# Kernel optimization log

Measured on AMD Instinct MI355X. Metric: run time of the kernel, lower is better.

The kernel has to match this reference:

```python
import jax, jax.numpy as jnp
import numpy as np
from jax import lax

B, T, HW = 8, 32, 128
D, NH, DEPTH, DFF = 384, 6, 6, 1536
PR = PC = 4
P = PR * PC
EPS = 1e-5


def _ln(x, g, b):
    mu = x.mean(-1, keepdims=True)
    v = ((x - mu) ** 2).mean(-1, keepdims=True)
    return (x - mu) / jnp.sqrt(v + EPS) * g + b


def _conv2d(x, w, s, p):
    return lax.conv_general_dilated(x, w, (s, s), [(p, p), (p, p)],
                                    dimension_numbers=('NCHW', 'OIHW', 'NCHW'))


def _bn(x, g, b, m, v):
    inv = g / jnp.sqrt(v + EPS)
    return x * inv[:, None, None] + (b - m * inv)[:, None, None]


def _gelu(x):
    return jax.nn.gelu(x, approximate=False)


def _forward(frames, conv1_w, bn1_g, bn1_b, bn1_m, bn1_v,
             conv2_w, bn2_g, bn2_b, bn2_m, bn2_v,
             conv3_w, bn3_g, bn3_b, bn3_m, bn3_v, proj_w,
             dw_w, dw_b, pw_w, pw_b, tnorm_g, tnorm_b,
             frame_pos, patch_pos, cls_token, cls_pos,
             qkv_w, qkv_b, out_w, out_b, ln1_g, ln1_b, ln2_g, ln2_b,
             ffn_w1, ffn_b1, ffn_w2, ffn_b2,
             head_ln_g, head_ln_b, head_w1, head_b1, head_w2, head_b2):
    b, t = frames.shape[0], frames.shape[1]
    # ---- FrameEncoder (eval-mode BN) ----
    x = frames.reshape(b * t, 1, HW, HW)
    x = _gelu(_bn(_conv2d(x, conv1_w, 2, 2), bn1_g, bn1_b, bn1_m, bn1_v))
    x = _gelu(_bn(_conv2d(x, conv2_w, 2, 1), bn2_g, bn2_b, bn2_m, bn2_v))
    x = _gelu(_bn(_conv2d(x, conv3_w, 2, 1), bn3_g, bn3_b, bn3_m, bn3_v))
    n, c, hh, ww = x.shape
    # adaptive avg pool (16,16)->(4,4) is an exact 4x4 mean pool
    x = x.reshape(n, c, PR, hh // PR, PC, ww // PC).mean(axis=(3, 5))
    x = jnp.einsum('oc,nchw->nohw', proj_w[:, :, 0, 0], x)  # 1x1 conv proj
    tokens = x.reshape(n, D, P).transpose(0, 2, 1).reshape(b, t, P, D)
    # ---- TemporalConvBlock (per-patch sequences) ----
    tc = tokens.transpose(0, 2, 1, 3).reshape(b * P, t, D)
    out = tc.transpose(0, 2, 1)  # [N, D, t]
    for i, dil in enumerate((1, 2)):
        pad = dil * (3 - 1) // 2
        h = lax.conv_general_dilated(out, dw_w[i], (1,), [(pad, pad)],
                                     rhs_dilation=(dil,), feature_group_count=D,
                                     dimension_numbers=('NCH', 'OIH', 'NCH'))
        h = _gelu(h + dw_b[i][None, :, None])
        h = jnp.einsum('oi,nit->not', pw_w[i], h) + pw_b[i][None, :, None]
        out = h + out
    out = out.transpose(0, 2, 1)
    tc = _ln(out + tc, tnorm_g, tnorm_b)
    tokens = tc.reshape(b, P, t, D).transpose(0, 2, 1, 3)
    # ---- positional + cls ----
    fp = frame_pos[:t].transpose(1, 0, 2)[:, :, None, :]  # [1,t,1,D]
    pp = patch_pos[:, None, :, :]                          # [1,1,P,D]
    tok = (tokens + fp + pp).reshape(b, t * P, D)
    cls = cls_token + cls_pos
    tok = jnp.concatenate([jnp.broadcast_to(cls, (b, 1, D)), tok], axis=1)
    S = t * P + 1
    # ---- block-structured additive mask (faithful to _build_causal_mask) ----
    ids = jnp.repeat(jnp.arange(t), P)
    neg = jnp.finfo(jnp.float32).min
    base = jnp.where(ids[None, :] < ids[:, None], neg, 0.0)
    mask = jnp.zeros((S, S), jnp.float32).at[1:, 1:].set(base).at[1:, 0].set(neg)
    # ---- pre-norm transformer encoder ----
    hd = D // NH
    scale = 1.0 / jnp.sqrt(jnp.float32(hd))
    x = tok
    for i in range(DEPTH):
        h = _ln(x, ln1_g[i], ln1_b[i])
        qkv = h @ qkv_w[i].T + qkv_b[i]
        q, k, v = jnp.split(qkv, 3, axis=-1)
        q = q.reshape(b, S, NH, hd).transpose(0, 2, 1, 3)
        k = k.reshape(b, S, NH, hd).transpose(0, 2, 1, 3)
        v = v.reshape(b, S, NH, hd).transpose(0, 2, 1, 3)
        scores = jnp.einsum('bhqd,bhkd->bhqk', q, k) * scale + mask
        a = jax.nn.softmax(scores, axis=-1)
        o = jnp.einsum('bhqk,bhkd->bhqd', a, v).transpose(0, 2, 1, 3).reshape(b, S, D)
        x = x + (o @ out_w[i].T + out_b[i])
        h2 = _ln(x, ln2_g[i], ln2_b[i])
        x = x + _gelu(h2 @ ffn_w1[i].T + ffn_b1[i]) @ ffn_w2[i].T + ffn_b2[i]
    # ---- coord head ----
    pooled = x[:, 0]
    h = _ln(pooled, head_ln_g, head_ln_b)
    h = _gelu(h @ head_w1.T + head_b1)
    coords = jax.nn.sigmoid(h @ head_w2.T + head_b2)
    return coords


def setup_inputs():
    ks = iter(jax.random.split(jax.random.key(0), 64))

    def r(shape, s):
        return jax.random.normal(next(ks), shape, jnp.float32) * s

    inp = {}
    inp['frames'] = jax.random.normal(next(ks), (B, T, 1, HW, HW), jnp.float32)
    inp['conv1_w'] = r((32, 1, 5, 5), 0.2)
    inp['bn1_g'] = jnp.ones(32); inp['bn1_b'] = jnp.zeros(32)
    inp['bn1_m'] = r((32,), 0.1)
    inp['bn1_v'] = jax.random.uniform(next(ks), (32,), jnp.float32, 0.5, 1.5)
    inp['conv2_w'] = r((64, 32, 3, 3), 0.1)
    inp['bn2_g'] = jnp.ones(64); inp['bn2_b'] = jnp.zeros(64)
    inp['bn2_m'] = r((64,), 0.1)
    inp['bn2_v'] = jax.random.uniform(next(ks), (64,), jnp.float32, 0.5, 1.5)
    inp['conv3_w'] = r((128, 64, 3, 3), 0.07)
    inp['bn3_g'] = jnp.ones(128); inp['bn3_b'] = jnp.zeros(128)
    inp['bn3_m'] = r((128,), 0.1)
    inp['bn3_v'] = jax.random.uniform(next(ks), (128,), jnp.float32, 0.5, 1.5)
    inp['proj_w'] = r((D, 128, 1, 1), 0.08)
    inp['dw_w'] = r((2, D, 1, 3), 0.3)
    inp['dw_b'] = jnp.zeros((2, D))
    inp['pw_w'] = r((2, D, D), 0.05)
    inp['pw_b'] = jnp.zeros((2, D))
    inp['tnorm_g'] = jnp.ones(D); inp['tnorm_b'] = jnp.zeros(D)
    inp['frame_pos'] = r((T, 1, D), 0.02)
    inp['patch_pos'] = r((1, P, D), 0.02)
    inp['cls_token'] = jnp.zeros((1, 1, D))
    inp['cls_pos'] = r((1, 1, D), 0.02)
    inp['qkv_w'] = r((DEPTH, 3 * D, D), 0.02)
    inp['qkv_b'] = jnp.zeros((DEPTH, 3 * D))
    inp['out_w'] = r((DEPTH, D, D), 0.02)
    inp['out_b'] = jnp.zeros((DEPTH, D))
    inp['ln1_g'] = jnp.ones((DEPTH, D)); inp['ln1_b'] = jnp.zeros((DEPTH, D))
    inp['ln2_g'] = jnp.ones((DEPTH, D)); inp['ln2_b'] = jnp.zeros((DEPTH, D))
    inp['ffn_w1'] = r((DEPTH, DFF, D), 0.02)
    inp['ffn_b1'] = jnp.zeros((DEPTH, DFF))
    inp['ffn_w2'] = r((DEPTH, D, DFF), 0.02)
    inp['ffn_b2'] = jnp.zeros((DEPTH, D))
    inp['head_ln_g'] = jnp.ones(D); inp['head_ln_b'] = jnp.zeros(D)
    inp['head_w1'] = r((D, D), 0.02); inp['head_b1'] = jnp.zeros(D)
    inp['head_w2'] = r((2, D), 0.02); inp['head_b2'] = jnp.zeros(2)
    return inp


def reference(frames, conv1_w, bn1_g, bn1_b, bn1_m, bn1_v,
              conv2_w, bn2_g, bn2_b, bn2_m, bn2_v,
              conv3_w, bn3_g, bn3_b, bn3_m, bn3_v, proj_w,
              dw_w, dw_b, pw_w, pw_b, tnorm_g, tnorm_b,
              frame_pos, patch_pos, cls_token, cls_pos,
              qkv_w, qkv_b, out_w, out_b, ln1_g, ln1_b, ln2_g, ln2_b,
              ffn_w1, ffn_b1, ffn_w2, ffn_b2,
              head_ln_g, head_ln_b, head_w1, head_b1, head_w2, head_b2):
    return _forward(frames, conv1_w, bn1_g, bn1_b, bn1_m, bn1_v,
                    conv2_w, bn2_g, bn2_b, bn2_m, bn2_v,
                    conv3_w, bn3_g, bn3_b, bn3_m, bn3_v, proj_w,
                    dw_w, dw_b, pw_w, pw_b, tnorm_g, tnorm_b,
                    frame_pos, patch_pos, cls_token, cls_pos,
                    qkv_w, qkv_b, out_w, out_b, ln1_g, ln1_b, ln2_g, ln2_b,
                    ffn_w1, ffn_b1, ffn_w2, ffn_b2,
                    head_ln_g, head_ln_b, head_w1, head_b1, head_w2, head_b2)
```

## Files before the change

### kernel.cpp

```cpp
#include <hip/hip_runtime.h>
#include <hip/hip_fp16.h>
#include <cstddef>

#define EPSV 1e-5f
#define SPLITS 4

typedef _Float16 f16;
typedef _Float16 f16x8 __attribute__((ext_vector_type(8)));
typedef float f32x4v __attribute__((ext_vector_type(4)));

__device__ __forceinline__ float gelu_f(float x) {
    return 0.5f * x * (1.0f + erff(x * 0.7071067811865476f));
}

__device__ __forceinline__ float gelu_fast(float x) {
    float x2 = x * x;
    float z = x * fmaf(0.10296103f, x2, 2.3025851f);
    float e = exp2f(z);
    float r = __builtin_amdgcn_rcpf(e + 1.0f);
    return fmaf(-x, r, x);
}

__global__ __launch_bounds__(256) void cvt_all_kernel(
    const float* __restrict__ p0, const float* __restrict__ p1,
// ... 162 lines not shown
        f16x8 b0 = *(const f16x8*)(&Bs[(wc + l15) * 40 + l4 * 8]);
        f16x8 b1 = *(const f16x8*)(&Bs[(wc + 16 + l15) * 40 + l4 * 8]);
        acc[0][0] = __builtin_amdgcn_mfma_f32_16x16x32_f16(a0, b0, acc[0][0], 0, 0, 0);
        acc[0][1] = __builtin_amdgcn_mfma_f32_16x16x32_f16(a0, b1, acc[0][1], 0, 0, 0);
        acc[1][0] = __builtin_amdgcn_mfma_f32_16x16x32_f16(a1, b0, acc[1][0], 0, 0, 0);
        acc[1][1] = __builtin_amdgcn_mfma_f32_16x16x32_f16(a1, b1, acc[1][1], 0, 0, 0);
    }
    float inv[2], beta[2];
    #pragma unroll
    for (int ni = 0; ni < 2; ni++) {
        int col = bn + wc + ni * 16 + l15;
        float iv = g[col] * rsqrtf(vr[col] + EPSV);
        inv[ni] = iv; beta[ni] = bt[col] - mn[col] * iv;
    }
    #pragma unroll
    for (int mi = 0; mi < 2; mi++) {
        #pragma unroll
        for (int q = 0; q < 4; q++) {
            int pixel = bm + wr + mi * 16 + l4 * 4 + q;
            #pragma unroll
            for (int ni = 0; ni < 2; ni++) {
                int col = bn + wc + ni * 16 + l15;
                float v = acc[mi][ni][q] * inv[ni] + beta[ni];
                out[(size_t)pixel * CO + col] = (f16)gelu_fast(v);
            }
        }
    }
}

__global__ __launch_bounds__(256) void poolh_kernel(
    const f16* __restrict__ in, f16* __restrict__ out, int NC)
{
    int idx = blockIdx.x * 256 + threadIdx.x;
    if (idx >= NC * 16 * 16) return;
    int cc = idx & 15; int npl = idx >> 4;
    int c0 = cc * 8;
    int n = npl >> 4; int p = npl & 15;
    int ph = p >> 2, pw = p & 3;
    const f16* base = in + (((size_t)(n * 16 + ph * 4)) * 16 + pw * 4) * 128 + c0;
    float s[8] = {};
    #pragma unroll
    for (int dy = 0; dy < 4; dy++)
        #pragma unroll
        for (int dx = 0; dx < 4; dx++) {
            f16x8 v = *(const f16x8*)(base + (dy * 16 + dx) * 128);
            #pragma unroll
            for (int u = 0; u < 8; u++) s[u] += (float)v[u];
        }
    f16* op = out + (size_t)npl * 128 + c0;
    #pragma unroll
    for (int u = 0; u < 8; u++) op[u] = (f16)(s[u] * 0.0625f);
}

template<int OUTF16, int ACT, int VTRANS, int TCMAP>
__global__ __launch_bounds__(256) void gemm_k64_kernel(
    const f16* __restrict__ A, const f16* __restrict__ B,
    const float* __restrict__ bias, const float* __restrict__ res,
    void* __restrict__ Cv, f16* __restrict__ vT, int M, int N, int K, int nrow)
{
    __shared__ __align__(16) f16 As[64 * 72];
    __shared__ __align__(16) f16 Bs[64 * 72];
    int nb = gridDim.x;
    int q = nb >> 3, r = nb & 7;
    int xcd = blockIdx.x & 7, pos = blockIdx.x >> 3;
    int logical = (xcd < r ? xcd * (q + 1) : r * (q + 1) + (xcd - r) * q) + pos;
    int brow = logical % nrow, bcol = logical / nrow;
    int bm = brow * 64, bn = bcol * 64;

    int tid = threadIdx.x;
    int lrow = tid >> 2, lseg = (tid & 3) * 16;
    int w = tid >> 6, lane = tid & 63;
    int wr = (w >> 1) * 32, wc = (w & 1) * 32;
    int l15 = lane & 15, l4 = lane >> 4;
    f32x4v zero = {0.f, 0.f, 0.f, 0.f};
    f32x4v acc[2][2];
    acc[0][0] = zero; acc[0][1] = zero; acc[1][0] = zero; acc[1][1] = zero;

    int arow = bm + lrow;
    bool aok = (arow < M);
    const f16* ap = A + (size_t)arow * K + lseg;
    const f16* bp = B + (size_t)(bn + lrow) * K + lseg;

    uint4 ra0 = make_uint4(0u,0u,0u,0u), ra1 = ra0, rb0, rb1;
    if (aok) { ra0 = *(const uint4*)(ap); ra1 = *(const uint4*)(ap + 8); }
    rb0 = *(const uint4*)(bp); rb1 = *(const uint4*)(bp + 8);

    int nt = K >> 6;
    for (int t = 0; t < nt; t++) {
        __syncthreads();
        *(uint4*)(&As[lrow * 72 + lseg])     = ra0;
        *(uint4*)(&As[lrow * 72 + lseg + 8]) = ra1;
        *(uint4*)(&Bs[lrow * 72 + lseg])     = rb0;
        *(uint4*)(&Bs[lrow * 72 + lseg + 8]) = rb1;
        if (t + 1 < nt) {
            int k0 = (t + 1) << 6;
            if (aok) { ra0 = *(const uint4*)(ap + k0); ra1 = *(const uint4*)(ap + k0 + 8); }
            rb0 = *(const uint4*)(bp + k0); rb1 = *(const uint4*)(bp + k0 + 8);
        }
        __syncthreads();
        #pragma unroll
        for (int s = 0; s < 2; s++) {
            f16x8 a0 = *(const f16x8*)(&As[(wr + l15) * 72 + s * 32 + l4 * 8]);
            f16x8 a1 = *(const f16x8*)(&As[(wr + 16 + l15) * 72 + s * 32 + l4 * 8]);
            f16x8 b0 = *(const f16x8*)(&Bs[(wc + l15) * 72 + s * 32 + l4 * 8]);
            f16x8 b1 = *(const f16x8*)(&Bs[(wc + 16 + l15) * 72 + s * 32 + l4 * 8]);
            acc[0][0] = __builtin_amdgcn_mfma_f32_16x16x32_f16(a0, b0, acc[0][0], 0, 0, 0);
            acc[0][1] = __builtin_amdgcn_mfma_f32_16x16x32_f16(a0, b1, acc[0][1], 0, 0, 0);
            acc[1][0] = __builtin_amdgcn_mfma_f32_16x16x32_f16(a1, b0, acc[1][0], 0, 0, 0);
            acc[1][1] = __builtin_amdgcn_mfma_f32_16x16x32_f16(a1, b1, acc[1][1], 0, 0, 0);
        }
    }

    if (VTRANS && bn >= 768) {
        __syncthreads();
        f16* tile = As;
        #pragma unroll
        for (int mi = 0; mi < 2; mi++)
            #pragma unroll
            for (int qq = 0; qq < 4; qq++) {
                int rl = wr + mi * 16 + l4 * 4 + qq;
                #pragma unroll
                for (int ni = 0; ni < 2; ni++) {
                    int dl = wc + ni * 16 + l15;
                    float v = acc[mi][ni][qq] + bias[bn + dl];
                    tile[dl * 66 + rl] = (f16)v;
                }
            }
        __syncthreads();
        int h = (bn - 768) >> 6;
        int j = tid & 63, dbase = tid >> 6;
        int trow = bm + j;
        if (trow < M) {
            int b = trow / 513;
            int jj = trow - b * 513;
            f16* vb = vT + ((size_t)(b * 6 + h) * 64) * 576 + jj;
            #pragma unroll
            for (int it = 0; it < 16; it++) {
                int d = dbase * 16 + it;
                vb[(size_t)d * 576] = tile[d * 66 + j];
            }
        }
        return;
    }
    #pragma unroll
    for (int mi = 0; mi < 2; mi++) {
        #pragma unroll
        for (int qq = 0; qq < 4; qq++) {
            int row = bm + wr + mi * 16 + l4 * 4 + qq;
            if (row >= M) continue;
            #pragma unroll
            for (int ni = 0; ni < 2; ni++) {
                int col = bn + wc + ni * 16 + l15;
                float v = acc[mi][ni][qq];
                if (bias) v += bias[col];
                if (ACT == 1) v = gelu_fast(v);
                if (res) v += res[(size_t)row * N + col];
                int orow = row;
                if (TCMAP) orow = (row & ~511) | ((row & 15) << 5) | ((row >> 4) & 31);
                if (OUTF16) ((f16*)Cv)[(size_t)orow * N + col] = (f16)v;
                else ((float*)Cv)[(size_t)orow * N + col] = v;
            }
        }
    }
}

template<int ACT>
__global__ __launch_bounds__(256) void gemm_kn128_kernel(
    const f16* __restrict__ A, const f16* __restrict__ B,
    const float* __restrict__ bias, f16* __restrict__ C,
    int M, int N, int K, int nrow)
{
    __shared__ __align__(16) f16 As[64 * 72];
    __shared__ __align__(16) f16 Bs[128 * 72];
    int nb = gridDim.x;
    int q = nb >> 3, r = nb & 7;
    int xcd = blockIdx.x & 7, pos = blockIdx.x >> 3;
    int logical = (xcd < r ? xcd * (q + 1) : r * (q + 1) + (xcd - r) * q) + pos;
    int brow = logical % nrow, bcol = logical / nrow;
    int bm = brow * 64, bn = bcol * 128;

    int tid = threadIdx.x;
    int w = tid >> 6, lane = tid & 63;
    int wr = (w >> 1) * 32, wc = (w & 1) * 64;
    int l15 = lane & 15, l4 = lane >> 4;
    int alrow = tid >> 2, alseg = (tid & 3) * 16;
    int blrow = tid >> 1, blseg = (tid & 1) * 32;

    f32x4v zero = {0.f, 0.f, 0.f, 0.f};
    f32x4v acc[2][4];
    #pragma unroll
    for (int i = 0; i < 2; i++)
        #pragma unroll
        for (int j = 0; j < 4; j++) acc[i][j] = zero;

    int arow = bm + alrow;
    bool aok = (arow < M);
    const f16* ap = A + (size_t)arow * K + alseg;
    const f16* bp = B + (size_t)(bn + blrow) * K + blseg;

    uint4 ra0 = make_uint4(0u,0u,0u,0u), ra1 = ra0;
    uint4 rb0, rb1, rb2, rb3;
    if (aok) { ra0 = *(const uint4*)(ap); ra1 = *(const uint4*)(ap + 8); }
    rb0 = *(const uint4*)(bp);      rb1 = *(const uint4*)(bp + 8);
    rb2 = *(const uint4*)(bp + 16); rb3 = *(const uint4*)(bp + 24);

    int ntiles = K >> 6;
    for (int t = 0; t < ntiles; t++) {
        __syncthreads();
        *(uint4*)(&As[alrow * 72 + alseg])     = ra0;
        *(uint4*)(&As[alrow * 72 + alseg + 8]) = ra1;
        *(uint4*)(&Bs[blrow * 72 + blseg])      = rb0;
        *(uint4*)(&Bs[blrow * 72 + blseg + 8])  = rb1;
        *(uint4*)(&Bs[blrow * 72 + blseg + 16]) = rb2;
        *(uint4*)(&Bs[blrow * 72 + blseg + 24]) = rb3;
        if (t + 1 < ntiles) {
            int k0 = (t + 1) << 6;
            if (aok) { ra0 = *(const uint4*)(ap + k0); ra1 = *(const uint4*)(ap + k0 + 8); }
            rb0 = *(const uint4*)(bp + k0);      rb1 = *(const uint4*)(bp + k0 + 8);
            rb2 = *(const uint4*)(bp + k0 + 16); rb3 = *(const uint4*)(bp + k0 + 24);
        }
        __syncthreads();
        #pragma unroll
        for (int s = 0; s < 2; s++) {
            f16x8 a0 = *(const f16x8*)(&As[(wr + l15) * 72 + s * 32 + l4 * 8]);
            f16x8 a1 = *(const f16x8*)(&As[(wr + 16 + l15) * 72 + s * 32 + l4 * 8]);
            #pragma unroll
            for (int j = 0; j < 4; j++) {
                f16x8 bf = *(const f16x8*)(&Bs[(wc + j * 16 + l15) * 72 + s * 32 + l4 * 8]);
                acc[0][j] = __builtin_amdgcn_mfma_f32_16x16x32_f16(a0, bf, acc[0][j], 0, 0, 0);
                acc[1][j] = __builtin_amdgcn_mfma_f32_16x16x32_f16(a1, bf, acc[1][j], 0, 0, 0);
            }
        }
    }
    #pragma unroll
    for (int mi = 0; mi < 2; mi++) {
        #pragma unroll
        for (int qq = 0; qq < 4; qq++) {
            int row = bm + wr + mi * 16 + l4 * 4 + qq;
            if (row >= M) continue;
            #pragma unroll
            for (int j = 0; j < 4; j++) {
                int col = bn + wc + j * 16 + l15;
                float v = acc[mi][j][qq];
                if (bias) v += bias[col];
                if (ACT == 1) v = gelu_fast(v);
                C[(size_t)row * N + col] = (f16)v;
            }
        }
    }
}

__global__ __launch_bounds__(256) void dwconv_kernel(
    const float* __restrict__ in, const float* __restrict__ w,
    const float* __restrict__ bias, f16* __restrict__ out, int dil)
{
    int idx = blockIdx.x * 256 + threadIdx.x;
    if (idx >= 128 * 32 * 384) return;
    int d = idx % 384; int t = (idx / 384) & 31; int s = idx / (384 * 32);
    const float* ip = in + (size_t)s * 32 * 384 + d;
    float acc = bias[d];
    #pragma unroll
    for (int k = 0; k < 3; k++) {
        int tt = t + (k - 1) * dil;
        if ((unsigned)tt < 32u) acc += w[d * 3 + k] * ip[tt * 384];
    }
    out[idx] = (f16)gelu_fast(acc);
}

__global__ __launch_bounds__(256) void ln_wave_kernel(
    const float* __restrict__ in,
    const float* __restrict__ g, const float* __restrict__ b,
    f16* __restrict__ out, int rows)
{
    int w = threadIdx.x >> 6, lane = threadIdx.x & 63;
    int row = blockIdx.x * 4 + w;
    if (row >= rows) return;
    const float* ip = in + (size_t)row * 384;
    float x[6]; float s = 0.f, s2 = 0.f;
    #pragma unroll
    for (int k = 0; k < 6; k++) {
        float v = ip[lane + 64 * k];
        x[k] = v; s += v; s2 += v * v;
    }
    #pragma unroll
    for (int off = 1; off < 64; off <<= 1) {
        s += __shfl_xor(s, off); s2 += __shfl_xor(s2, off);
    }
    float mu = s * (1.f / 384.f);
    float var = s2 * (1.f / 384.f) - mu * mu;
    float rs = rsqrtf(var + EPSV);
    #pragma unroll
    for (int k = 0; k < 6; k++) {
        int c = lane + 64 * k;
        out[(size_t)row * 384 + c] = (f16)((x[k] - mu) * rs * g[c] + b[c]);
    }
}

__global__ __launch_bounds__(128) void build_x_kernel(
    const float* __restrict__ mix, const float* __restrict__ tc,
    const float* __restrict__ tg, const float* __restrict__ tb,
    const float* __restrict__ fpos, const float* __restrict__ ppos,
    float* __restrict__ x)
{
    int row = blockIdx.x;
    int t = row & 31; int bp = row >> 5;
    int p = bp & 15; int b = bp >> 4;
    int tid = threadIdx.x;
    const float* ip = mix + (size_t)row * 384;
    const float* ip2 = tc + (size_t)row * 384;
    __shared__ float red[128], red2[128];
    float v[3]; float s = 0.f, s2 = 0.f;
    #pragma unroll
    for (int j = 0; j < 3; j++) {
        float val = ip[tid + 128 * j] + ip2[tid + 128 * j];
        v[j] = val; s += val; s2 += val * val;
    }
    red[tid] = s; red2[tid] = s2; __syncthreads();
    for (int off = 64; off >= 1; off >>= 1) {
        if (tid < off) { red[tid] += red[tid + off]; red2[tid] += red2[tid + off]; }
        __syncthreads();
    }
    float mu = red[0] * (1.f / 384.f);
    float var = red2[0] * (1.f / 384.f) - mu * mu;
    float rs = rsqrtf(var + EPSV);
    size_t xbase = ((size_t)b * 513 + 1 + t * 16 + p) * 384;
    #pragma unroll
    for (int j = 0; j < 3; j++) {
        int c = tid + 128 * j;
        float y = (v[j] - mu) * rs * tg[c] + tb[c] + fpos[t * 384 + c] + ppos[p * 384 + c];
        x[xbase + c] = y;
    }
}

__global__ __launch_bounds__(256) void cls_kernel(
    const float* __restrict__ ct, const float* __restrict__ cp, float* __restrict__ x)
{
    int idx = blockIdx.x * 256 + threadIdx.x;
    if (idx >= 8 * 384) return;
    int c = idx % 384; int b = idx / 384;
    x[(size_t)b * 513 * 384 + c] = ct[c] + cp[c];
}

__global__ __launch_bounds__(256) void fattn_split_kernel(
    const f16* __restrict__ qkv, const f16* __restrict__ vT,
    f16* __restrict__ Op, float* __restrict__ ml)
{
    __shared__ __align__(16) f16 Pl[4][16][72];
    int qt = blockIdx.x;
// ... 75 lines not shown
                float sv = valid ? S[jf][r] * 0.125f : -INFINITY;
                pj[jf][r] = sv;
                mx = fmaxf(mx, sv);
            }
            mx = fmaxf(mx, __shfl_xor(mx, 1));
            mx = fmaxf(mx, __shfl_xor(mx, 2));
            mx = fmaxf(mx, __shfl_xor(mx, 4));
            mx = fmaxf(mx, __shfl_xor(mx, 8));
            float mn = fmaxf(m[r], mx);
            float alpha = (m[r] == -INFINITY) ? 0.f : __expf(m[r] - mn);
            float ls = 0.f;
            #pragma unroll
            for (int jf = 0; jf < 4; jf++) {
                float p = (pj[jf][r] == -INFINITY) ? 0.f : __expf(pj[jf][r] - mn);
                pj[jf][r] = p; ls += p;
            }
            ls += __shfl_xor(ls, 1); ls += __shfl_xor(ls, 2);
            ls += __shfl_xor(ls, 4); ls += __shfl_xor(ls, 8);
            l[r] = alpha * l[r] + ls;
            m[r] = mn;
            #pragma unroll
            for (int df = 0; df < 4; df++) O[df][r] *= alpha;
        }
        #pragma unroll
        for (int jf = 0; jf < 4; jf++)
            #pragma unroll
            for (int r = 0; r < 4; r++)
                Pl[w][4 * g + r][jf * 16 + l15] = (f16)pj[jf][r];
        #pragma unroll
        for (int s = 0; s < 2; s++) {
            f16x8 pf = *(const f16x8*)(&Pl[w][l15][s * 32 + g * 8]);
            #pragma unroll
            for (int df = 0; df < 4; df++)
                O[df] = __builtin_amdgcn_mfma_f32_16x16x32_f16(pf, vreg[s * 4 + df], O[df], 0, 0, 0);
        }
        #pragma unroll
        for (int i = 0; i < 8; i++) kreg[i] = knext[i];
    }

    int rowbase = third * 24624 + bh * 513;
    #pragma unroll
    for (int r = 0; r < 4; r++) {
        int qi = q0w + 4 * g + r;
        if (qi > 512) continue;
        size_t ro = (size_t)(rowbase + qi);
        #pragma unroll
        for (int df = 0; df < 4; df++)
            Op[ro * 64 + df * 16 + l15] = (f16)O[df][r];
        if (l15 == 0) {
            ml[ro * 2 + 0] = m[r];
            ml[ro * 2 + 1] = l[r];
        }
    }
}

__global__ __launch_bounds__(256) void attn_combine_kernel(
    const f16* __restrict__ Op, const float* __restrict__ ml,
    f16* __restrict__ ob)
{
    int row = blockIdx.x * 4 + (threadIdx.x >> 6);
    if (row >= 24624) return;
    int lane = threadIdx.x & 63;
    int bh = row / 513, qi = row - bh * 513;
    int b = bh / 6, h = bh - b * 6;
    float mv[SPLITS], lv[SPLITS], mm = -INFINITY;
    #pragma unroll
    for (int s = 0; s < SPLITS; s++) {
        mv[s] = ml[((size_t)s * 24624 + row) * 2];
        lv[s] = ml[((size_t)s * 24624 + row) * 2 + 1];
        mm = fmaxf(mm, mv[s]);
    }
    float onum = 0.f, lden = 0.f;
    #pragma unroll
    for (int s = 0; s < SPLITS; s++) {
        float a = (mv[s] == -INFINITY) ? 0.f : __expf(mv[s] - mm);
        lden += lv[s] * a;
        onum += (float)Op[((size_t)s * 24624 + row) * 64 + lane] * a;
    }
    ob[((size_t)(b * 513 + qi)) * 384 + h * 64 + lane] = (f16)(onum / lden);
}

__global__ __launch_bounds__(384) void head_kernel(
    const float* __restrict__ x, const float* __restrict__ lg, const float* __restrict__ lb,
    const float* __restrict__ w1, const float* __restrict__ b1,
    const float* __restrict__ w2, const float* __restrict__ b2,
    float* __restrict__ out)
{
    int b = blockIdx.x; int t = threadIdx.x;
    __shared__ float hs[384], h1[384];
    __shared__ float rs[6], rs2[6];
    const float* xp = x + (size_t)b * 513 * 384;
    float v = xp[t];
    float s = v, s2 = v * v;
    #pragma unroll
    for (int off = 32; off >= 1; off >>= 1) {
        s += __shfl_down(s, off); s2 += __shfl_down(s2, off);
    }
    if ((t & 63) == 0) { rs[t >> 6] = s; rs2[t >> 6] = s2; }
    __syncthreads();
    float S = 0.f, S2 = 0.f;
    #pragma unroll
    for (int i = 0; i < 6; i++) { S += rs[i]; S2 += rs2[i]; }
    float mu = S * (1.f / 384.f);
    float var = S2 * (1.f / 384.f) - mu * mu;
    float rstd = rsqrtf(var + EPSV);
    hs[t] = (v - mu) * rstd * lg[t] + lb[t];
    __syncthreads();
    const float* wr = w1 + (size_t)t * 384;
    float acc = b1[t];
    for (int c = 0; c < 384; c += 4) {
        float4 w4 = *reinterpret_cast<const float4*>(wr + c);
        acc += w4.x * hs[c] + w4.y * hs[c + 1] + w4.z * hs[c + 2] + w4.w * hs[c + 3];
    }
    h1[t] = gelu_f(acc);
    __syncthreads();
    float p0 = h1[t] * w2[t], p1 = h1[t] * w2[384 + t];
    #pragma unroll
    for (int off = 32; off >= 1; off >>= 1) {
        p0 += __shfl_down(p0, off); p1 += __shfl_down(p1, off);
    }
    if ((t & 63) == 0) { rs[t >> 6] = p0; rs2[t >> 6] = p1; }
    __syncthreads();
    if (t == 0) {
        float a0 = b2[0], a1 = b2[1];
        #pragma unroll
        for (int i = 0; i < 6; i++) { a0 += rs[i]; a1 += rs2[i]; }
        out[b * 2 + 0] = 1.f / (1.f + expf(-a0));
        out[b * 2 + 1] = 1.f / (1.f + expf(-a1));
    }
}

static inline int cdiv(int a, int b) { return (a + b - 1) / b; }
// ... 8 lines not shown
    const float* bn1_m = (const float*)d_in[4]; const float* bn1_v = (const float*)d_in[5];
    const float* conv2_w = (const float*)d_in[6];
    const float* bn2_g = (const float*)d_in[7]; const float* bn2_b = (const float*)d_in[8];
    const float* bn2_m = (const float*)d_in[9]; const float* bn2_v = (const float*)d_in[10];
    const float* conv3_w = (const float*)d_in[11];
    const float* bn3_g = (const float*)d_in[12]; const float* bn3_b = (const float*)d_in[13];
    const float* bn3_m = (const float*)d_in[14]; const float* bn3_v = (const float*)d_in[15];
    const float* proj_w = (const float*)d_in[16];
    const float* dw_w = (const float*)d_in[17]; const float* dw_b = (const float*)d_in[18];
    const float* pw_w = (const float*)d_in[19]; const float* pw_b = (const float*)d_in[20];
    const float* tnorm_g = (const float*)d_in[21]; const float* tnorm_b = (const float*)d_in[22];
    const float* frame_pos = (const float*)d_in[23];
    const float* patch_pos = (const float*)d_in[24];
    const float* cls_token = (const float*)d_in[25];
    const float* cls_pos = (const float*)d_in[26];
    const float* qkv_w = (const float*)d_in[27]; const float* qkv_b = (const float*)d_in[28];
    const float* out_w = (const float*)d_in[29]; const float* out_b = (const float*)d_in[30];
    const float* ln1_g = (const float*)d_in[31]; const float* ln1_b = (const float*)d_in[32];
    const float* ln2_g = (const float*)d_in[33]; const float* ln2_b = (const float*)d_in[34];
    const float* ffn_w1 = (const float*)d_in[35]; const float* ffn_b1 = (const float*)d_in[36];
    const float* ffn_w2 = (const float*)d_in[37]; const float* ffn_b2 = (const float*)d_in[38];
    const float* head_ln_g = (const float*)d_in[39]; const float* head_ln_b = (const float*)d_in[40];
    const float* head_w1 = (const float*)d_in[41]; const float* head_b1 = (const float*)d_in[42];
    const float* head_w2 = (const float*)d_in[43]; const float* head_b2 = (const float*)d_in[44];
    (void)in_sizes; (void)n_in; (void)out_size; (void)ws_size;

    char* base = (char*)d_ws;
    size_t off = 0;
    auto alloc = [&](size_t bytes) { void* p = base + off; off = (off + bytes + 255) & ~(size_t)255; return p; };

    f16* wtotal = (f16*)alloc((size_t)10960896 * 2);
    f16* projw16 = wtotal;
    f16* pw16    = wtotal + 49152;
    f16* qkvw16  = wtotal + 344064;
    f16* outw16  = wtotal + 2998272;
    f16* f1w16   = wtotal + 3883008;
    f16* f2w16   = wtotal + 7421952;
    f16* c1wB    = (f16*)alloc(1024 * 2);
    f16* c2w16   = (f16*)alloc((size_t)64 * 288 * 2);
    f16* c3w16   = (f16*)alloc((size_t)128 * 576 * 2);
    f16* pooled  = (f16*)alloc((size_t)4096 * 128 * 2);
    float* tc    = (float*)alloc((size_t)4096 * 384 * 4);

    size_t ustart = off;
    f16* c1h = (f16*)alloc((size_t)256 * 64 * 64 * 32 * 2);
    f16* c2h = (f16*)alloc((size_t)256 * 32 * 32 * 64 * 2);
    f16* c3h = (f16*)alloc((size_t)256 * 16 * 16 * 128 * 2);
    size_t uend_stem = off;
    off = ustart;
    float* mA = (float*)alloc((size_t)4096 * 384 * 4);
    float* mB = (float*)alloc((size_t)4096 * 384 * 4);
    f16*   mh = (f16*)alloc((size_t)4096 * 384 * 2);
    float* xb   = (float*)alloc((size_t)8 * 513 * 384 * 4);
    f16*   hb   = (f16*)alloc((size_t)8 * 513 * 384 * 2);
    f16*   qkvb = (f16*)alloc((size_t)8 * 513 * 1152 * 2);
    f16*   vTb  = (f16*)alloc((size_t)48 * 64 * 576 * 2);
    f16*   ob   = (f16*)alloc((size_t)8 * 513 * 384 * 2);
    f16*   ffb  = (f16*)alloc((size_t)8 * 513 * 1536 * 2);
    f16*   Opart = (f16*)alloc((size_t)SPLITS * 24624 * 64 * 2);
    float* mlpart = (float*)alloc((size_t)SPLITS * 24624 * 2 * 4);
    if (off < uend_stem) off = uend_stem;

    cvt_all_kernel<<<4096, 256, 0, stream>>>(
        proj_w, pw_w, qkv_w, out_w, ffn_w1, ffn_w2, wtotal);
    conv1_w_prep_kernel<<<4, 256, 0, stream>>>(conv1_w, bn1_g, bn1_v, c1wB);
    conv_w_reorder_kernel<<<cdiv(64 * 288, 256), 256, 0, stream>>>(conv2_w, c2w16, 64, 32);
    conv_w_reorder_kernel<<<cdiv(128 * 576, 256), 256, 0, stream>>>(conv3_w, c3w16, 128, 64);

    conv1_mfma_kernel<<<256 * 16, 256, 0, stream>>>(
        frames, c1wB, bn1_b, bn1_m, bn1_g, bn1_v, c1h);
    convg_kernel<32, 64, 64><<<dim3(4096, 1), 256, 0, stream>>>(
        c1h, c2w16, bn2_g, bn2_b, bn2_m, bn2_v, c2h);
    convg_kernel<64, 32, 128><<<dim3(1024, 2), 256, 0, stream>>>(
        c2h, c3w16, bn3_g, bn3_b, bn3_m, bn3_v, c3h);
    poolh_kernel<<<256, 256, 0, stream>>>(c3h, pooled, 256);
    gemm_k64_kernel<0, 0, 0, 1><<<384, 256, 0, stream>>>(
        pooled, projw16, nullptr, nullptr, tc, nullptr, 4096, 384, 128, 64);

    dwconv_kernel<<<cdiv(128 * 32 * 384, 256), 256, 0, stream>>>(
        tc, dw_w, dw_b, mh, 1);
    gemm_k64_kernel<0, 0, 0, 0><<<384, 256, 0, stream>>>(
        mh, pw16, pw_b, tc, mA, nullptr, 4096, 384, 384, 64);
    dwconv_kernel<<<cdiv(128 * 32 * 384, 256), 256, 0, stream>>>(
        mA, dw_w + 384 * 3, dw_b + 384, mh, 2);
    gemm_k64_kernel<0, 0, 0, 0><<<384, 256, 0, stream>>>(
        mh, pw16 + 384 * 384, pw_b + 384, mA, mB, nullptr, 4096, 384, 384, 64);

    build_x_kernel<<<128 * 32, 128, 0, stream>>>(
        mB, tc, tnorm_g, tnorm_b, frame_pos, patch_pos, xb);
    cls_kernel<<<cdiv(8 * 384, 256), 256, 0, stream>>>(cls_token, cls_pos, xb);

    const int M = 8 * 513;
    const int NR = cdiv(M, 64);
    for (int l = 0; l < 6; l++) {
        ln_wave_kernel<<<cdiv(M, 4), 256, 0, stream>>>(xb,
            ln1_g + (size_t)l * 384, ln1_b + (size_t)l * 384, hb, M);
        gemm_k64_kernel<1, 0, 1, 0><<<NR * 18, 256, 0, stream>>>(
            hb, qkvw16 + (size_t)l * 1152 * 384, qkv_b + (size_t)l * 1152,
            nullptr, qkvb, vTb, M, 1152, 384, NR);
        fattn_split_kernel<<<dim3(9, 48, SPLITS), 256, 0, stream>>>(qkvb, vTb, Opart, mlpart);
        attn_combine_kernel<<<cdiv(24624, 4), 256, 0, stream>>>(Opart, mlpart, ob);
        gemm_k64_kernel<0, 0, 0, 0><<<NR * 6, 256, 0, stream>>>(
            ob, outw16 + (size_t)l * 384 * 384, out_b + (size_t)l * 384,
            xb, xb, nullptr, M, 384, 384, NR);
        ln_wave_kernel<<<cdiv(M, 4), 256, 0, stream>>>(xb,
            ln2_g + (size_t)l * 384, ln2_b + (size_t)l * 384, hb, M);
        gemm_kn128_kernel<1><<<NR * 12, 256, 0, stream>>>(
            hb, f1w16 + (size_t)l * 1536 * 384, ffn_b1 + (size_t)l * 1536,
            ffb, M, 1536, 384, NR);
        gemm_k64_kernel<0, 0, 0, 0><<<NR * 6, 256, 0, stream>>>(
            ffb, f2w16 + (size_t)l * 384 * 1536, ffn_b2 + (size_t)l * 384,
            xb, xb, nullptr, M, 384, 1536, NR);
    }

    head_kernel<<<8, 384, 0, stream>>>(
        xb, head_ln_g, head_ln_b, head_w1, head_b1, head_w2, head_b2, (float*)d_out);
}
```

Baseline: 836.0 us.

## Fuse LayerNorm into QKV/FFN1 GEMMs and attention combine into out-proj GEMM

LayerNorm is now computed inside the GEMM prologue. Each block normalizes its 64 rows of the fp32 residual stream and keeps the full 64x384 fp16 A tile resident in shared memory. The split-attention combine is likewise folded into the output-projection GEMM's A-tile construction, which removes three kernels per layer and the hb/ob intermediate round-trips. In exchange, each column block recomputes LN or the combine redundantly (18-24 times for LN, 6 for the combine), uses about 59KB of shared memory per block, and FFN1 moves from 64x128 to 64x64 tiles.

```diff
diff --git a/kernel.cpp b/kernel.cpp
--- a/kernel.cpp
+++ b/kernel.cpp
@@ -238,11 +238,11 @@
     for (int u = 0; u < 8; u++) op[u] = (f16)(s[u] * 0.0625f);
 }
 
-template<int OUTF16, int ACT, int VTRANS, int TCMAP>
+template<int OUTF16, int ACT, int TCMAP>
 __global__ __launch_bounds__(256) void gemm_k64_kernel(
     const f16* __restrict__ A, const f16* __restrict__ B,
     const float* __restrict__ bias, const float* __restrict__ res,
-    void* __restrict__ Cv, f16* __restrict__ vT, int M, int N, int K, int nrow)
+    void* __restrict__ Cv, int M, int N, int K, int nrow)
 {
     __shared__ __align__(16) f16 As[64 * 72];
     __shared__ __align__(16) f16 Bs[64 * 72];
@@ -297,37 +297,6 @@
         }
     }
 
-    if (VTRANS && bn >= 768) {
-        __syncthreads();
-        f16* tile = As;
-        #pragma unroll
-        for (int mi = 0; mi < 2; mi++)
-            #pragma unroll
-            for (int qq = 0; qq < 4; qq++) {
-                int rl = wr + mi * 16 + l4 * 4 + qq;
-                #pragma unroll
-                for (int ni = 0; ni < 2; ni++) {
-                    int dl = wc + ni * 16 + l15;
-                    float v = acc[mi][ni][qq] + bias[bn + dl];
-                    tile[dl * 66 + rl] = (f16)v;
-                }
-            }
-        __syncthreads();
-        int h = (bn - 768) >> 6;
-        int j = tid & 63, dbase = tid >> 6;
-        int trow = bm + j;
-        if (trow < M) {
-            int b = trow / 513;
-            int jj = trow - b * 513;
-            f16* vb = vT + ((size_t)(b * 6 + h) * 64) * 576 + jj;
-            #pragma unroll
-            for (int it = 0; it < 16; it++) {
-                int d = dbase * 16 + it;
-                vb[(size_t)d * 576] = tile[d * 66 + j];
-            }
-        }
-        return;
-    }
     #pragma unroll
     for (int mi = 0; mi < 2; mi++) {
         #pragma unroll
@@ -350,73 +319,124 @@
     }
 }
 
-template<int ACT>
-__global__ __launch_bounds__(256) void gemm_kn128_kernel(
-    const f16* __restrict__ A, const f16* __restrict__ B,
-    const float* __restrict__ bias, f16* __restrict__ C,
-    int M, int N, int K, int nrow)
-{
-    __shared__ __align__(16) f16 As[64 * 72];
-    __shared__ __align__(16) f16 Bs[128 * 72];
+template<int ACT, int VTRANS>
+__global__ __launch_bounds__(256) void gemm_ln_kernel(
+    const float* __restrict__ Xf, const float* __restrict__ lng, const float* __restrict__ lnb,
+    const f16* __restrict__ B, const float* __restrict__ bias,
+    f16* __restrict__ C, f16* __restrict__ vT, int M, int N, int nrow)
+{
+    __shared__ __align__(16) f16 As[64 * 392];
+    __shared__ __align__(16) f16 Bs[64 * 72];
     int nb = gridDim.x;
     int q = nb >> 3, r = nb & 7;
     int xcd = blockIdx.x & 7, pos = blockIdx.x >> 3;
     int logical = (xcd < r ? xcd * (q + 1) : r * (q + 1) + (xcd - r) * q) + pos;
     int brow = logical % nrow, bcol = logical / nrow;
-    int bm = brow * 64, bn = bcol * 128;
+    int bm = brow * 64, bn = bcol * 64;
 
     int tid = threadIdx.x;
+    int lrow = tid >> 2, g = tid & 3;
+    int lseg = g * 16;
     int w = tid >> 6, lane = tid & 63;
-    int wr = (w >> 1) * 32, wc = (w & 1) * 64;
+    int wr = (w >> 1) * 32, wc = (w & 1) * 32;
     int l15 = lane & 15, l4 = lane >> 4;
-    int alrow = tid >> 2, alseg = (tid & 3) * 16;
-    int blrow = tid >> 1, blseg = (tid & 1) * 32;
+
+    int arow = bm + lrow;
+    bool aok = (arow < M);
+    const float* xp = Xf + (size_t)arow * 384;
+    float s = 0.f, s2 = 0.f;
+    if (aok) {
+        #pragma unroll
+        for (int k = 0; k < 6; k++)
+            #pragma unroll
+            for (int j = 0; j < 4; j++) {
+                float4 v = *(const float4*)(xp + k * 64 + lseg + j * 4);
+                s += v.x + v.y + v.z + v.w;
+                s2 += v.x * v.x + v.y * v.y + v.z * v.z + v.w * v.w;
+            }
+    }
+    s += __shfl_xor(s, 1); s += __shfl_xor(s, 2);
+    s2 += __shfl_xor(s2, 1); s2 += __shfl_xor(s2, 2);
+    float mu = s * (1.f / 384.f);
+    float var = s2 * (1.f / 384.f) - mu * mu;
+    float rs = rsqrtf(var + EPSV);
+    #pragma unroll
+    for (int k = 0; k < 6; k++) {
+        f16 tmp[16];
+        #pragma unroll
+        for (int j = 0; j < 4; j++) {
+            int c = k * 64 + lseg + j * 4;
+            float4 v = aok ? *(const float4*)(xp + c) : make_float4(0.f, 0.f, 0.f, 0.f);
+            float4 gg = *(const float4*)(lng + c);
+            float4 bb = *(const float4*)(lnb + c);
+            tmp[j * 4 + 0] = (f16)((v.x - mu) * rs * gg.x + bb.x);
+            tmp[j * 4 + 1] = (f16)((v.y - mu) * rs * gg.y + bb.y);
+            tmp[j * 4 + 2] = (f16)((v.z - mu) * rs * gg.z + bb.z);
+            tmp[j * 4 + 3] = (f16)((v.w - mu) * rs * gg.w + bb.w);
+        }
+        *(uint4*)(&As[lrow * 392 + k * 64 + lseg])     = *(uint4*)(tmp);
+        *(uint4*)(&As[lrow * 392 + k * 64 + lseg + 8]) = *(uint4*)(tmp + 8);
+    }
+
+    const f16* bp = B + (size_t)(bn + lrow) * 384 + lseg;
+    uint4 rb0 = *(const uint4*)(bp), rb1 = *(const uint4*)(bp + 8);
+    __syncthreads();
 
     f32x4v zero = {0.f, 0.f, 0.f, 0.f};
-    f32x4v acc[2][4];
-    #pragma unroll
-    for (int i = 0; i < 2; i++)
-        #pragma unroll
-        for (int j = 0; j < 4; j++) acc[i][j] = zero;
-
-    int arow = bm + alrow;
-    bool aok = (arow < M);
-    const f16* ap = A + (size_t)arow * K + alseg;
-    const f16* bp = B + (size_t)(bn + blrow) * K + blseg;
-
-    uint4 ra0 = make_uint4(0u,0u,0u,0u), ra1 = ra0;
-    uint4 rb0, rb1, rb2, rb3;
-    if (aok) { ra0 = *(const uint4*)(ap); ra1 = *(const uint4*)(ap + 8); }
-    rb0 = *(const uint4*)(bp);      rb1 = *(const uint4*)(bp + 8);
-    rb2 = *(const uint4*)(bp + 16); rb3 = *(const uint4*)(bp + 24);
-
-    int ntiles = K >> 6;
-    for (int t = 0; t < ntiles; t++) {
+    f32x4v acc[2][2];
+    acc[0][0] = zero; acc[0][1] = zero; acc[1][0] = zero; acc[1][1] = zero;
+
+    for (int t = 0; t < 6; t++) {
+        *(uint4*)(&Bs[lrow * 72 + lseg])     = rb0;
+        *(uint4*)(&Bs[lrow * 72 + lseg + 8]) = rb1;
+        if (t < 5) {
+            rb0 = *(const uint4*)(bp + (t + 1) * 64);
+            rb1 = *(const uint4*)(bp + (t + 1) * 64 + 8);
+        }
         __syncthreads();
-        *(uint4*)(&As[alrow * 72 + alseg])     = ra0;
-        *(uint4*)(&As[alrow * 72 + alseg + 8]) = ra1;
-        *(uint4*)(&Bs[blrow * 72 + blseg])      = rb0;
-        *(uint4*)(&Bs[blrow * 72 + blseg + 8])  = rb1;
-        *(uint4*)(&Bs[blrow * 72 + blseg + 16]) = rb2;
-        *(uint4*)(&Bs[blrow * 72 + blseg + 24]) = rb3;
-        if (t + 1 < ntiles) {
-            int k0 = (t + 1) << 6;
-            if (aok) { ra0 = *(const uint4*)(ap + k0); ra1 = *(const uint4*)(ap + k0 + 8); }
-            rb0 = *(const uint4*)(bp + k0);      rb1 = *(const uint4*)(bp + k0 + 8);
-            rb2 = *(const uint4*)(bp + k0 + 16); rb3 = *(const uint4*)(bp + k0 + 24);
+        #pragma unroll
+        for (int ss = 0; ss < 2; ss++) {
+            f16x8 a0 = *(const f16x8*)(&As[(wr + l15) * 392 + t * 64 + ss * 32 + l4 * 8]);
+            f16x8 a1 = *(const f16x8*)(&As[(wr + 16 + l15) * 392 + t * 64 + ss * 32 + l4 * 8]);
+            f16x8 b0 = *(const f16x8*)(&Bs[(wc + l15) * 72 + ss * 32 + l4 * 8]);
+            f16x8 b1 = *(const f16x8*)(&Bs[(wc + 16 + l15) * 72 + ss * 32 + l4 * 8]);
+            acc[0][0] = __builtin_amdgcn_mfma_f32_16x16x32_f16(a0, b0, acc[0][0], 0, 0, 0);
+            acc[0][1] = __builtin_amdgcn_mfma_f32_16x16x32_f16(a0, b1, acc[0][1], 0, 0, 0);
+            acc[1][0] = __builtin_amdgcn_mfma_f32_16x16x32_f16(a1, b0, acc[1][0], 0, 0, 0);
+            acc[1][1] = __builtin_amdgcn_mfma_f32_16x16x32_f16(a1, b1, acc[1][1], 0, 0, 0);
         }
         __syncthreads();
-        #pragma unroll
-        for (int s = 0; s < 2; s++) {
-            f16x8 a0 = *(const f16x8*)(&As[(wr + l15) * 72 + s * 32 + l4 * 8]);
-            f16x8 a1 = *(const f16x8*)(&As[(wr + 16 + l15) * 72 + s * 32 + l4 * 8]);
-            #pragma unroll
-            for (int j = 0; j < 4; j++) {
-                f16x8 bf = *(const f16x8*)(&Bs[(wc + j * 16 + l15) * 72 + s * 32 + l4 * 8]);
-                acc[0][j] = __builtin_amdgcn_mfma_f32_16x16x32_f16(a0, bf, acc[0][j], 0, 0, 0);
-                acc[1][j] = __builtin_amdgcn_mfma_f32_16x16x32_f16(a1, bf, acc[1][j], 0, 0, 0);
-            }
-        }
+    }
+
+    if (VTRANS && bn >= 768) {
+        f16* tile = As;
+        #pragma unroll
+        for (int mi = 0; mi < 2; mi++)
+            #pragma unroll
+            for (int qq = 0; qq < 4; qq++) {
+                int rl = wr + mi * 16 + l4 * 4 + qq;
+                #pragma unroll
+                for (int ni = 0; ni < 2; ni++) {
+                    int dl = wc + ni * 16 + l15;
+                    float v = acc[mi][ni][qq] + bias[bn + dl];
+                    tile[dl * 66 + rl] = (f16)v;
+                }
+            }
+        __syncthreads();
+        int h = (bn - 768) >> 6;
+        int j = tid & 63, dbase = tid >> 6;
+        int trow = bm + j;
+        if (trow < M) {
+            int b = trow / 513;
+            int jj = trow - b * 513;
+            f16* vb = vT + ((size_t)(b * 6 + h) * 64) * 576 + jj;
+            #pragma unroll
+            for (int it = 0; it < 16; it++) {
+                int d = dbase * 16 + it;
+                vb[(size_t)d * 576] = tile[d * 66 + j];
+            }
+        }
+        return;
     }
     #pragma unroll
     for (int mi = 0; mi < 2; mi++) {
@@ -425,12 +445,123 @@
             int row = bm + wr + mi * 16 + l4 * 4 + qq;
             if (row >= M) continue;
             #pragma unroll
-            for (int j = 0; j < 4; j++) {
-                int col = bn + wc + j * 16 + l15;
-                float v = acc[mi][j][qq];
-                if (bias) v += bias[col];
+            for (int ni = 0; ni < 2; ni++) {
+                int col = bn + wc + ni * 16 + l15;
+                float v = acc[mi][ni][qq] + bias[col];
                 if (ACT == 1) v = gelu_fast(v);
                 C[(size_t)row * N + col] = (f16)v;
+            }
+        }
+    }
+}
+
+__global__ __launch_bounds__(256) void gemm_comb_kernel(
+    const f16* __restrict__ Op, const float* __restrict__ ml,
+    const f16* __restrict__ B, const float* __restrict__ bias,
+    float* __restrict__ xio, int M, int nrow)
+{
+    __shared__ __align__(16) f16 As[64 * 392];
+    __shared__ __align__(16) f16 Bs[64 * 72];
+    int nb = gridDim.x;
+    int q = nb >> 3, r = nb & 7;
+    int xcd = blockIdx.x & 7, pos = blockIdx.x >> 3;
+    int logical = (xcd < r ? xcd * (q + 1) : r * (q + 1) + (xcd - r) * q) + pos;
+    int brow = logical % nrow, bcol = logical / nrow;
+    int bm = brow * 64, bn = bcol * 64;
+
+    int tid = threadIdx.x;
+    int lrow = tid >> 2, g = tid & 3;
+    int lseg = g * 16;
+    int w = tid >> 6, lane = tid & 63;
+    int wr = (w >> 1) * 32, wc = (w & 1) * 32;
+    int l15 = lane & 15, l4 = lane >> 4;
+
+    int arow = bm + lrow;
+    bool aok = (arow < M);
+    int b = aok ? arow / 513 : 0;
+    int qi = arow - b * 513;
+    #pragma unroll
+    for (int h = 0; h < 6; h++) {
+        f16 tmp[16];
+        if (aok) {
+            size_t oprow = (size_t)(b * 6 + h) * 513 + qi;
+            float mv[SPLITS], lv[SPLITS], mm = -INFINITY;
+            #pragma unroll
+            for (int sp = 0; sp < SPLITS; sp++) {
+                mv[sp] = ml[((size_t)sp * 24624 + oprow) * 2];
+                lv[sp] = ml[((size_t)sp * 24624 + oprow) * 2 + 1];
+                mm = fmaxf(mm, mv[sp]);
+            }
+            float sc[SPLITS], lden = 0.f;
+            #pragma unroll
+            for (int sp = 0; sp < SPLITS; sp++) {
+                float a = (mv[sp] == -INFINITY) ? 0.f : __expf(mv[sp] - mm);
+                sc[sp] = a; lden += lv[sp] * a;
+            }
+            float rl = 1.0f / lden;
+            float accv[16] = {};
+            #pragma unroll
+            for (int sp = 0; sp < SPLITS; sp++) {
+                f16x8 o0 = *(const f16x8*)(Op + ((size_t)sp * 24624 + oprow) * 64 + lseg);
+                f16x8 o1 = *(const f16x8*)(Op + ((size_t)sp * 24624 + oprow) * 64 + lseg + 8);
+                #pragma unroll
+                for (int e = 0; e < 8; e++) {
+                    accv[e]     = fmaf((float)o0[e], sc[sp], accv[e]);
+                    accv[e + 8] = fmaf((float)o1[e], sc[sp], accv[e + 8]);
+                }
+            }
+            #pragma unroll
+            for (int e = 0; e < 16; e++) tmp[e] = (f16)(accv[e] * rl);
+        } else {
+            #pragma unroll
+            for (int e = 0; e < 16; e++) tmp[e] = (f16)0.f;
+        }
+        *(uint4*)(&As[lrow * 392 + h * 64 + lseg])     = *(uint4*)(tmp);
+        *(uint4*)(&As[lrow * 392 + h * 64 + lseg + 8]) = *(uint4*)(tmp + 8);
+    }
+
+    const f16* bp = B + (size_t)(bn + lrow) * 384 + lseg;
+    uint4 rb0 = *(const uint4*)(bp), rb1 = *(const uint4*)(bp + 8);
+    __syncthreads();
+
+    f32x4v zero = {0.f, 0.f, 0.f, 0.f};
+    f32x4v acc[2][2];
+    acc[0][0] = zero; acc[0][1] = zero; acc[1][0] = zero; acc[1][1] = zero;
+
+    for (int t = 0; t < 6; t++) {
+        *(uint4*)(&Bs[lrow * 72 + lseg])     = rb0;
+        *(uint4*)(&Bs[lrow * 72 + lseg + 8]) = rb1;
+        if (t < 5) {
+            rb0 = *(const uint4*)(bp + (t + 1) * 64);
+            rb1 = *(const uint4*)(bp + (t + 1) * 64 + 8);
+        }
+        __syncthreads();
+        #pragma unroll
+        for (int ss = 0; ss < 2; ss++) {
+            f16x8 a0 = *(const f16x8*)(&As[(wr + l15) * 392 + t * 64 + ss * 32 + l4 * 8]);
+            f16x8 a1 = *(const f16x8*)(&As[(wr + 16 + l15) * 392 + t * 64 + ss * 32 + l4 * 8]);
+            f16x8 b0 = *(const f16x8*)(&Bs[(wc + l15) * 72 + ss * 32 + l4 * 8]);
+            f16x8 b1 = *(const f16x8*)(&Bs[(wc + 16 + l15) * 72 + ss * 32 + l4 * 8]);
+            acc[0][0] = __builtin_amdgcn_mfma_f32_16x16x32_f16(a0, b0, acc[0][0], 0, 0, 0);
+            acc[0][1] = __builtin_amdgcn_mfma_f32_16x16x32_f16(a0, b1, acc[0][1], 0, 0, 0);
+            acc[1][0] = __builtin_amdgcn_mfma_f32_16x16x32_f16(a1, b0, acc[1][0], 0, 0, 0);
+            acc[1][1] = __builtin_amdgcn_mfma_f32_16x16x32_f16(a1, b1, acc[1][1], 0, 0, 0);
+        }
+        __syncthreads();
+    }
+
+    #pragma unroll
+    for (int mi = 0; mi < 2; mi++) {
+        #pragma unroll
+        for (int qq = 0; qq < 4; qq++) {
+            int row = bm + wr + mi * 16 + l4 * 4 + qq;
+            if (row >= M) continue;
+            #pragma unroll
+            for (int ni = 0; ni < 2; ni++) {
+                int col = bn + wc + ni * 16 + l15;
+                float v = acc[mi][ni][qq] + bias[col];
+                v += xio[(size_t)row * 384 + col];
+                xio[(size_t)row * 384 + col] = v;
             }
         }
     }
@@ -451,35 +582,6 @@
         if ((unsigned)tt < 32u) acc += w[d * 3 + k] * ip[tt * 384];
     }
     out[idx] = (f16)gelu_fast(acc);
-}
-
-__global__ __launch_bounds__(256) void ln_wave_kernel(
-    const float* __restrict__ in,
-    const float* __restrict__ g, const float* __restrict__ b,
-    f16* __restrict__ out, int rows)
-{
-    int w = threadIdx.x >> 6, lane = threadIdx.x & 63;
-    int row = blockIdx.x * 4 + w;
-    if (row >= rows) return;
-    const float* ip = in + (size_t)row * 384;
-    float x[6]; float s = 0.f, s2 = 0.f;
-    #pragma unroll
-    for (int k = 0; k < 6; k++) {
-        float v = ip[lane + 64 * k];
-        x[k] = v; s += v; s2 += v * v;
-    }
-    #pragma unroll
-    for (int off = 1; off < 64; off <<= 1) {
-        s += __shfl_xor(s, off); s2 += __shfl_xor(s2, off);
-    }
-    float mu = s * (1.f / 384.f);
-    float var = s2 * (1.f / 384.f) - mu * mu;
-    float rs = rsqrtf(var + EPSV);
-    #pragma unroll
-    for (int k = 0; k < 6; k++) {
-        int c = lane + 64 * k;
-        out[(size_t)row * 384 + c] = (f16)((x[k] - mu) * rs * g[c] + b[c]);
-    }
 }
 
 __global__ __launch_bounds__(128) void build_x_kernel(
@@ -661,32 +763,6 @@
             ml[ro * 2 + 1] = l[r];
         }
     }
-}
-
-__global__ __launch_bounds__(256) void attn_combine_kernel(
-    const f16* __restrict__ Op, const float* __restrict__ ml,
-    f16* __restrict__ ob)
-{
-    int row = blockIdx.x * 4 + (threadIdx.x >> 6);
-    if (row >= 24624) return;
-    int lane = threadIdx.x & 63;
-    int bh = row / 513, qi = row - bh * 513;
-    int b = bh / 6, h = bh - b * 6;
-    float mv[SPLITS], lv[SPLITS], mm = -INFINITY;
-    #pragma unroll
-    for (int s = 0; s < SPLITS; s++) {
-        mv[s] = ml[((size_t)s * 24624 + row) * 2];
-        lv[s] = ml[((size_t)s * 24624 + row) * 2 + 1];
-        mm = fmaxf(mm, mv[s]);
-    }
-    float onum = 0.f, lden = 0.f;
-    #pragma unroll
-    for (int s = 0; s < SPLITS; s++) {
-        float a = (mv[s] == -INFINITY) ? 0.f : __expf(mv[s] - mm);
-        lden += lv[s] * a;
-        onum += (float)Op[((size_t)s * 24624 + row) * 64 + lane] * a;
-    }
-    ob[((size_t)(b * 513 + qi)) * 384 + h * 64 + lane] = (f16)(onum / lden);
 }
 
 __global__ __launch_bounds__(384) void head_kernel(
@@ -801,10 +877,8 @@
     float* mB = (float*)alloc((size_t)4096 * 384 * 4);
     f16*   mh = (f16*)alloc((size_t)4096 * 384 * 2);
     float* xb   = (float*)alloc((size_t)8 * 513 * 384 * 4);
-    f16*   hb   = (f16*)alloc((size_t)8 * 513 * 384 * 2);
     f16*   qkvb = (f16*)alloc((size_t)8 * 513 * 1152 * 2);
     f16*   vTb  = (f16*)alloc((size_t)48 * 64 * 576 * 2);
-    f16*   ob   = (f16*)alloc((size_t)8 * 513 * 384 * 2);
     f16*   ffb  = (f16*)alloc((size_t)8 * 513 * 1536 * 2);
     f16*   Opart = (f16*)alloc((size_t)SPLITS * 24624 * 64 * 2);
     float* mlpart = (float*)alloc((size_t)SPLITS * 24624 * 2 * 4);
@@ -823,17 +897,17 @@
     convg_kernel<64, 32, 128><<<dim3(1024, 2), 256, 0, stream>>>(
         c2h, c3w16, bn3_g, bn3_b, bn3_m, bn3_v, c3h);
     poolh_kernel<<<256, 256, 0, stream>>>(c3h, pooled, 256);
-    gemm_k64_kernel<0, 0, 0, 1><<<384, 256, 0, stream>>>(
-        pooled, projw16, nullptr, nullptr, tc, nullptr, 4096, 384, 128, 64);
+    gemm_k64_kernel<0, 0, 1><<<384, 256, 0, stream>>>(
+        pooled, projw16, nullptr, nullptr, tc, 4096, 384, 128, 64);
 
     dwconv_kernel<<<cdiv(128 * 32 * 384, 256), 256, 0, stream>>>(
         tc, dw_w, dw_b, mh, 1);
-    gemm_k64_kernel<0, 0, 0, 0><<<384, 256, 0, stream>>>(
-        mh, pw16, pw_b, tc, mA, nullptr, 4096, 384, 384, 64);
+    gemm_k64_kernel<0, 0, 0><<<384, 256, 0, stream>>>(
+        mh, pw16, pw_b, tc, mA, 4096, 384, 384, 64);
     dwconv_kernel<<<cdiv(128 * 32 * 384, 256), 256, 0, stream>>>(
         mA, dw_w + 384 * 3, dw_b + 384, mh, 2);
-    gemm_k64_kernel<0, 0, 0, 0><<<384, 256, 0, stream>>>(
-        mh, pw16 + 384 * 384, pw_b + 384, mA, mB, nullptr, 4096, 384, 384, 64);
+    gemm_k64_kernel<0, 0, 0><<<384, 256, 0, stream>>>(
+        mh, pw16 + 384 * 384, pw_b + 384, mA, mB, 4096, 384, 384, 64);
 
     build_x_kernel<<<128 * 32, 128, 0, stream>>>(
         mB, tc, tnorm_g, tnorm_b, frame_pos, patch_pos, xb);
@@ -842,24 +916,21 @@
     const int M = 8 * 513;
     const int NR = cdiv(M, 64);
     for (int l = 0; l < 6; l++) {
-        ln_wave_kernel<<<cdiv(M, 4), 256, 0, stream>>>(xb,
-            ln1_g + (size_t)l * 384, ln1_b + (size_t)l * 384, hb, M);
-        gemm_k64_kernel<1, 0, 1, 0><<<NR * 18, 256, 0, stream>>>(
-            hb, qkvw16 + (size_t)l * 1152 * 384, qkv_b + (size_t)l * 1152,
-            nullptr, qkvb, vTb, M, 1152, 384, NR);
+        gemm_ln_kernel<0, 1><<<NR * 18, 256, 0, stream>>>(
+            xb, ln1_g + (size_t)l * 384, ln1_b + (size_t)l * 384,
+            qkvw16 + (size_t)l * 1152 * 384, qkv_b + (size_t)l * 1152,
+            qkvb, vTb, M, 1152, NR);
         fattn_split_kernel<<<dim3(9, 48, SPLITS), 256, 0, stream>>>(qkvb, vTb, Opart, mlpart);
-        attn_combine_kernel<<<cdiv(24624, 4), 256, 0, stream>>>(Opart, mlpart, ob);
-        gemm_k64_kernel<0, 0, 0, 0><<<NR * 6, 256, 0, stream>>>(
-            ob, outw16 + (size_t)l * 384 * 384, out_b + (size_t)l * 384,
-            xb, xb, nullptr, M, 384, 384, NR);
-        ln_wave_kernel<<<cdiv(M, 4), 256, 0, stream>>>(xb,
-            ln2_g + (size_t)l * 384, ln2_b + (size_t)l * 384, hb, M);
-        gemm_kn128_kernel<1><<<NR * 12, 256, 0, stream>>>(
-            hb, f1w16 + (size_t)l * 1536 * 384, ffn_b1 + (size_t)l * 1536,
-            ffb, M, 1536, 384, NR);
-        gemm_k64_kernel<0, 0, 0, 0><<<NR * 6, 256, 0, stream>>>(
+        gemm_comb_kernel<<<NR * 6, 256, 0, stream>>>(
+            Opart, mlpart, outw16 + (size_t)l * 384 * 384, out_b + (size_t)l * 384,
+            xb, M, NR);
+        gemm_ln_kernel<1, 0><<<NR * 24, 256, 0, stream>>>(
+            xb, ln2_g + (size_t)l * 384, ln2_b + (size_t)l * 384,
+            f1w16 + (size_t)l * 1536 * 384, ffn_b1 + (size_t)l * 1536,
+            ffb, nullptr, M, 1536, NR);
+        gemm_k64_kernel<0, 0, 0><<<NR * 6, 256, 0, stream>>>(
             ffb, f2w16 + (size_t)l * 384 * 1536, ffn_b2 + (size_t)l * 384,
-            xb, xb, nullptr, M, 384, 1536, NR);
+            xb, xb, M, 384, 1536, NR);
     }
 
     head_kernel<<<8, 384, 0, stream>>>(
```

Result: slower. 1.220 ms (+45.9%).
